# Performance work log

Hardware: AMD Instinct MI355X
Metric: run time of the kernel (lower is better)

Reference implementation:

```python
import jax, jax.numpy as jnp
import numpy as np

EPS = 1e-5  # eqx.nn.LayerNorm default


def _layer_norm(x, w, b):
    m = x.mean(-1, keepdims=True)
    v = ((x - m) ** 2).mean(-1, keepdims=True)
    return (x - m) / jnp.sqrt(v + EPS) * w + b


def _s4_block(x, nw, nb, lre, lim, bre, bim, cre, cim, d, lstep, ow, ob, o2w, o2b):
    # x: [L, H]. One SequenceBlock: LayerNorm -> S4 recurrence (lax.scan) -> GELU -> GLU-style gated linear -> residual.
    skip = x
    h = _layer_norm(x, nw, nb)
    Lam = lre + 1j * lim                      # [H, N] complex diagonal state matrix
    step = jnp.exp(lstep)[:, None]            # [H, 1] per-channel timescale
    BL = 1.0 / (1.0 - (step / 2.0) * Lam)     # bilinear discretization
    Abar = BL * (1.0 + (step / 2.0) * Lam)    # [H, N]
    Bbar = BL * step * (bre + 1j * bim)       # [H, N]
    C = cre + 1j * cim                        # [H, N]

    def scan_fn(state, u):                    # state: [H, N] complex, u: [H]
        new = Abar * state + Bbar * u[:, None]
        y = 2.0 * jnp.sum(C * new, axis=-1).real + d * u
        return new, y

    init = jnp.zeros(Abar.shape, Abar.dtype)  # cell.init_state
    _, y = jax.lax.scan(scan_fn, init, h)     # [L, H]
    y = jax.nn.gelu(y)
    y = (y @ ow.T + ob) * jax.nn.sigmoid(y @ o2w.T + o2b)
    return skip + y


def setup_inputs() -> dict:
    key = jax.random.key(0)
    L, IN, OUT, H, N, NL = 2048, 4, 3, 512, 32, 4
    ks = jax.random.split(key, 16)
    return {
        "x": jax.random.normal(ks[0], (L, IN), jnp.float32),
        "enc_w": jax.random.normal(ks[1], (H, IN), jnp.float32) / np.sqrt(IN),
        "enc_b": jnp.zeros((H,), jnp.float32),
        "dec_w": jax.random.normal(ks[2], (OUT, H), jnp.float32) / np.sqrt(H),
        "dec_b": jnp.zeros((OUT,), jnp.float32),
        "norm_w": jnp.ones((NL, H), jnp.float32),
        "norm_b": jnp.zeros((NL, H), jnp.float32),
        "lam_re": -0.5 - jax.random.uniform(ks[3], (NL, H, N), jnp.float32),  # stable (Re < 0)
        "lam_im": np.pi * jax.random.normal(ks[4], (NL, H, N), jnp.float32),
        "b_re": jax.random.normal(ks[5], (NL, H, N), jnp.float32) / np.sqrt(N),
        "b_im": jax.random.normal(ks[6], (NL, H, N), jnp.float32) / np.sqrt(N),
        "c_re": jax.random.normal(ks[7], (NL, H, N), jnp.float32) / np.sqrt(N),
        "c_im": jax.random.normal(ks[8], (NL, H, N), jnp.float32) / np.sqrt(N),
        "d": jax.random.normal(ks[9], (NL, H), jnp.float32),
        "log_step": float(np.log(1e-3)) + float(np.log(1e-1) - np.log(1e-3)) * jax.random.uniform(ks[10], (NL, H), jnp.float32),
        "out_w": jax.random.normal(ks[11], (NL, H, H), jnp.float32) / np.sqrt(H),
        "out_b": jnp.zeros((NL, H), jnp.float32),
        "out2_w": jax.random.normal(ks[12], (NL, H, H), jnp.float32) / np.sqrt(H),
        "out2_b": jnp.zeros((NL, H), jnp.float32),
    }


def reference(x, enc_w, enc_b, dec_w, dec_b, norm_w, norm_b, lam_re, lam_im, b_re, b_im, c_re, c_im, d, log_step, out_w, out_b, out2_w, out2_b):
    h = x @ enc_w.T + enc_b                   # encoder: [L, IN] -> [L, H]
    for i in range(norm_w.shape[0]):          # fixed small n_layers loop
        h = _s4_block(h, norm_w[i], norm_b[i], lam_re[i], lam_im[i], b_re[i], b_im[i],
                      c_re[i], c_im[i], d[i], log_step[i], out_w[i], out_b[i], out2_w[i], out2_b[i])
    return h @ dec_w.T + dec_b                # decoder: [L, H] -> [L, OUT]
```

## Files before the change

### kernel.cpp

```cpp
#include <hip/hip_runtime.h>
#include <hip/hip_bf16.h>
#include <math.h>

#define LSEQ 2048
#define HD   512
#define NST  32
#define LC   32
#define NCHK 64
#define NSUP 8
#define HH   (HD * HD)

typedef __bf16 bf16;
typedef __bf16 bf16x8 __attribute__((ext_vector_type(8)));
typedef float  floatx4 __attribute__((ext_vector_type(4)));

__device__ __forceinline__ float gelu_tanh(float x) {
    float z = 0.7978845608028654f * (x + 0.044715f * x * x * x);
    float e = __expf(2.f * z);
    float th = 1.f - 2.f / (e + 1.f);
    return 0.5f * x * (1.f + th);
}

__device__ __forceinline__ void make_ab(float lre, float lim, float step,
                                        float br0, float bi0,
                                        float& ar, float& ai, float& br, float& bi) {
    float s2 = 0.5f * step;
    float dr = 1.f - s2 * lre, di = -s2 * lim;
    float inv = 1.f / (dr * dr + di * di);
    float blr = dr * inv, bli = -di * inv;
    float nr = 1.f + s2 * lre, ni = s2 * lim;
    ar = blr * nr - bli * ni;
    ai = blr * ni + bli * nr;
    float tr = step * br0, ti = step * bi0;
    br = blr * tr - bli * ti;
    bi = blr * ti + bli * tr;
}

__global__ __launch_bounds__(256) void setup_kernel(
    const float* __restrict__ x,   const float* __restrict__ ew,
    const float* __restrict__ eb,  const float* __restrict__ ow,
    const float* __restrict__ o2w,
    const float* __restrict__ lre, const float* __restrict__ lim,
    const float* __restrict__ bre, const float* __restrict__ bim,
    const float* __restrict__ cre, const float* __restrict__ cim,
    const float* __restrict__ ls,
    float* __restrict__ h, bf16* __restrict__ wb,
    float2* __restrict__ cA, float2* __restrict__ cB,
    float2* __restrict__ cC, float2* __restrict__ cAp,
    float2* __restrict__ cApJ, float2* __restrict__ statP) {
    int bid = blockIdx.x, tid = threadIdx.x;
    if (bid < 4096) {
        int idx = bid * 256 + tid;
        int t = idx >> 9, col = idx & (HD - 1);
        float4 xv = *(const float4*)(x + t * 4);
        float4 wv = *(const float4*)(ew + col * 4);
        float acc = eb[col];
        acc = fmaf(xv.x, wv.x, acc); acc = fmaf(xv.y, wv.y, acc);
        acc = fmaf(xv.z, wv.z, acc); acc = fmaf(xv.w, wv.w, acc);
        h[idx] = acc;
        float s = acc, s2 = acc * acc;
#pragma unroll
        for (int m = 1; m <= 8; m <<= 1) {
            s  += __shfl_xor(s, m, 64);
            s2 += __shfl_xor(s2, m, 64);
        }
        if ((tid & 15) == 0) statP[(size_t)t * 32 + (col >> 4)] = make_float2(s, s2);
    } else if (bid < 5120) {
        int b2 = bid - 4096;
        const float* src = (b2 >= 512) ? o2w : ow;
        bf16* dst = wb + (b2 >= 512 ? 4 * HH : 0);
        int i = ((b2 & 511) * 256 + tid) * 8;
        float4 a = *(const float4*)(src + i);
        float4 b = *(const float4*)(src + i + 4);
        bf16x8 o;
        o[0] = (bf16)a.x; o[1] = (bf16)a.y; o[2] = (bf16)a.z; o[3] = (bf16)a.w;
        o[4] = (bf16)b.x; o[5] = (bf16)b.y; o[6] = (bf16)b.z; o[7] = (bf16)b.w;
        *(bf16x8*)(dst + i) = o;
    } else {
        int tg = (bid - 5120) * 256 + tid;
        int lay = tg >> 14, rem = tg & 16383;
        int ch = rem >> 5, n = rem & 31;
        float step = __expf(ls[lay * HD + ch]);
        float ar, ai, br, bi;
        make_ab(lre[tg], lim[tg], step, bre[tg], bim[tg], ar, ai, br, bi);
        float xr = ar, xi = ai;
#pragma unroll
        for (int q = 0; q < 5; ++q) { float tt = xr * xr - xi * xi; xi = 2.f * xr * xi; xr = tt; }
        int dst = (lay * NST + n) * HD + ch;
        cA[dst]  = make_float2(ar, ai);
        cB[dst]  = make_float2(br, bi);
        cC[dst]  = make_float2(2.f * cre[tg], 2.f * cim[tg]);
        cAp[dst] = make_float2(xr, xi);
        float pr = xr, pi = xi;
#pragma unroll
        for (int jj = 0; jj < 7; ++jj) {
            cApJ[((size_t)(lay * 7 + jj) * NST + n) * HD + ch] = make_float2(pr, pi);
            float t2r = pr * xr - pi * xi;
            float t2i = pr * xi + pi * xr;
            pr = t2r; pi = t2i;
        }
    }
}

__global__ __launch_bounds__(512, 1) void p1_kernel(
    const float* __restrict__ h, const float2* __restrict__ statP,
    const float* __restrict__ nwp, const float* __restrict__ nbp,
    const float2* __restrict__ cA, const float2* __restrict__ cB,
    const float2* __restrict__ cAp,
    float2* __restrict__ f, int lay) {
    __shared__ float tile[256 * 16];
    __shared__ float2 stat_s[256];
    __shared__ float2 fs[8 * 32 * 16];
    const int tid = threadIdx.x;
    const int lane = tid & 63, w = tid >> 6;
    const int chl = lane & 15, sub = lane >> 4;
    const int bx = blockIdx.x, sup = blockIdx.y;
    const int ch = bx * 16 + chl;

    const float* ub = h + (size_t)(sup * 256) * HD + bx * 16;
#pragma unroll
    for (int r = 0; r < 2; ++r) {
        int i = r * 512 + tid;
        int tr = i >> 2, c4 = (i & 3) * 4;
        *(float4*)(tile + tr * 16 + c4) = *(const float4*)(ub + (size_t)tr * HD + c4);
    }
    if (tid < 256) {
        const float4* pp = (const float4*)(statP + (size_t)(sup * 256 + tid) * 32);
        float S = 0.f, S2 = 0.f;
#pragma unroll
        for (int k = 0; k < 16; ++k) {
            float4 v = pp[k];
            S += v.x + v.z; S2 += v.y + v.w;
        }
        float m = S * (1.f / HD);
        float var = S2 * (1.f / HD) - m * m;
        stat_s[tid] = make_float2(m, rsqrtf(var + 1e-5f));
    }
    int cbase = (lay * NST + sub * 8) * HD + ch;
    float aR[8], aI[8], bR[8], bI[8];
#pragma unroll
    for (int j = 0; j < 8; ++j) {
        float2 t2 = cA[cbase + j * HD]; aR[j] = t2.x; aI[j] = t2.y;
        t2 = cB[cbase + j * HD];        bR[j] = t2.x; bI[j] = t2.y;
    }
    float gam = nwp[ch], bet = nbp[ch];
    __syncthreads();

    const float* tp = tile + (w * 32) * 16 + chl;
    float sr[8], si[8];
#pragma unroll
    for (int j = 0; j < 8; ++j) { sr[j] = 0.f; si[j] = 0.f; }
#pragma unroll 4
    for (int t = 0; t < LC; ++t) {
        float2 st = stat_s[w * 32 + t];
        float gr = gam * st.y;
        float off = fmaf(-st.x, gr, bet);
        float uu = fmaf(tp[t * 16], gr, off);
#pragma unroll
        for (int j = 0; j < 8; ++j) {
            float nr = fmaf(aR[j], sr[j], fmaf(-aI[j], si[j], bR[j] * uu));
            float ni = fmaf(aI[j], sr[j], fmaf( aR[j], si[j], bI[j] * uu));
            sr[j] = nr; si[j] = ni;
        }
    }
#pragma unroll
    for (int j = 0; j < 8; ++j)
        fs[(w * 32 + sub * 8 + j) * 16 + chl] = make_float2(sr[j], si[j]);
    __syncthreads();

    int n2 = tid >> 4, c2 = tid & 15;
    int chg = bx * 16 + c2;
    float2 ap = cAp[(lay * NST + n2) * HD + chg];
    const size_t CS = (size_t)NST * HD;
    float2* fo = f + (size_t)n2 * HD + chg;
    float s2r = 0.f, s2i = 0.f;
#pragma unroll
    for (int k = 0; k < 8; ++k) {
        float2 v = fs[(k * 32 + n2) * 16 + c2];
        float nr = fmaf(ap.x, s2r, fmaf(-ap.y, s2i, v.x));
        float ni = fmaf(ap.y, s2r, fmaf( ap.x, s2i, v.y));
        s2r = nr; s2i = ni;
        fo[(size_t)(sup * 8 + k) * CS] = make_float2(s2r, s2i);
    }
}

__global__ __launch_bounds__(256) void p2_kernel(
    const float2* __restrict__ f, const float2* __restrict__ cAp,
    float2* __restrict__ Sx, int lay) {
    int tg = blockIdx.x * 256 + threadIdx.x;
    int ch = tg & 511, n = tg >> 9;
    float2 ap = cAp[(lay * NST + n) * HD + ch];
    float xr = ap.x, xi = ap.y;
#pragma unroll
    for (int q = 0; q < 3; ++q) { float tt = xr * xr - xi * xi; xi = 2.f * xr * xi; xr = tt; }
    const size_t CS = (size_t)NST * HD;
    const float2* fp = f + (size_t)n * HD + ch;
    float2 F[8];
#pragma unroll
    for (int k = 0; k < 8; ++k) F[k] = fp[(size_t)(k * 8 + 7) * CS];
    float2* sp = Sx + (size_t)n * HD + ch;
    float sr = 0.f, si = 0.f;
#pragma unroll
    for (int k = 0; k < 8; ++k) {
        sp[(size_t)k * CS] = make_float2(sr, si);
        float nr = fmaf(xr, sr, fmaf(-xi, si, F[k].x));
        float ni = fmaf(xi, sr, fmaf( xr, si, F[k].y));
        sr = nr; si = ni;
    }
}

__global__ __launch_bounds__(256, 2) void p3_kernel(
    const float* __restrict__ h, const float2* __restrict__ statP,
    const float* __restrict__ nwp, const float* __restrict__ nbp,
    const float2* __restrict__ f, const float2* __restrict__ Sx,
    const float2* __restrict__ cApJ,
    const float2* __restrict__ cA, const float2* __restrict__ cB,
    const float2* __restrict__ cC, const float* __restrict__ d_p,
    bf16* __restrict__ g, int lay) {
    __shared__ float tile[128 * 16];
    __shared__ float2 stat_s[128];
    const int tid = threadIdx.x;
    const int lane = tid & 63, w = tid >> 6;
    const int chl = lane & 15, sub = lane >> 4;
    const int bx = blockIdx.x, by = blockIdx.y;
    const int ch = bx * 16 + chl;
    const int chunk = by * 4 + w;

    const float* ub = h + (size_t)(by * 128) * HD + bx * 16;
#pragma unroll
    for (int r = 0; r < 2; ++r) {
        int i = r * 256 + tid;
        int tr = i >> 2, c4 = (i & 3) * 4;
        *(float4*)(tile + tr * 16 + c4) = *(const float4*)(ub + (size_t)tr * HD + c4);
    }
    if (tid < 128) {
        const float4* pp = (const float4*)(statP + (size_t)(by * 128 + tid) * 32);
        float S = 0.f, S2 = 0.f;
#pragma unroll
        for (int k = 0; k < 16; ++k) {
            float4 v = pp[k];
            S += v.x + v.z; S2 += v.y + v.w;
        }
        float m = S * (1.f / HD);
        float var = S2 * (1.f / HD) - m * m;
        stat_s[tid] = make_float2(m, rsqrtf(var + 1e-5f));
    }
    int cbase = (lay * NST + sub * 8) * HD + ch;
    float aR[8], aI[8], bR[8], bI[8], cR[8], cI[8];
#pragma unroll
    for (int j = 0; j < 8; ++j) {
        float2 t2 = cA[cbase + j * HD]; aR[j] = t2.x; aI[j] = t2.y;
        t2 = cB[cbase + j * HD];        bR[j] = t2.x; bI[j] = t2.y;
        t2 = cC[cbase + j * HD];        cR[j] = t2.x; cI[j] = t2.y;
    }
    float dch = d_p[lay * HD + ch];
    float gam = nwp[ch], bet = nbp[ch];

    float sr[8], si[8];
    int jj = chunk & 7, ksup = chunk >> 3;
    if (chunk == 0) {
#pragma unroll
        for (int j = 0; j < 8; ++j) { sr[j] = 0.f; si[j] = 0.f; }
    } else if (jj == 0) {
        const float2* sp = Sx + ((size_t)ksup * NST + sub * 8) * HD + ch;
#pragma unroll
        for (int j = 0; j < 8; ++j) { float2 v = sp[(size_t)j * HD]; sr[j] = v.x; si[j] = v.y; }
    } else {
        const float2* fw = f + ((size_t)(chunk - 1) * NST + sub * 8) * HD + ch;
        const float2* sp = Sx + ((size_t)ksup * NST + sub * 8) * HD + ch;
        const float2* aj = cApJ + ((size_t)(lay * 7 + (jj - 1)) * NST + sub * 8) * HD + ch;
#pragma unroll
        for (int j = 0; j < 8; ++j) {
            float2 F = fw[(size_t)j * HD];
            float2 S = sp[(size_t)j * HD];
            float2 A = aj[(size_t)j * HD];
            sr[j] = fmaf(A.x, S.x, fmaf(-A.y, S.y, F.x));
            si[j] = fmaf(A.x, S.y, fmaf( A.y, S.x, F.y));
        }
    }
    __syncthreads();

    const float* tp = tile + (w * 32) * 16 + chl;
    bf16* gp = g + (size_t)chunk * LC * HD + ch;
#pragma unroll 4
    for (int t = 0; t < LC; ++t) {
        float2 st = stat_s[w * 32 + t];
        float gr = gam * st.y;
        float off = fmaf(-st.x, gr, bet);
        float uu = fmaf(tp[t * 16], gr, off);
        float p = 0.f;
#pragma unroll
        for (int j = 0; j < 8; ++j) {
            float nr = fmaf(aR[j], sr[j], fmaf(-aI[j], si[j], bR[j] * uu));
            float ni = fmaf(aI[j], sr[j], fmaf( aR[j], si[j], bI[j] * uu));
            sr[j] = nr; si[j] = ni;
            p = fmaf(cR[j], nr, fmaf(-cI[j], ni, p));
        }
        p += __shfl_xor(p, 16);
        p += __shfl_xor(p, 32);
        float y = fmaf(dch, uu, p);
        if (sub == 0) gp[(size_t)t * HD] = (bf16)gelu_tanh(y);
    }
}

__global__ __launch_bounds__(256, 2) void mm_kernel(
    const bf16* __restrict__ A,
    const bf16* __restrict__ W1,
    const bf16* __restrict__ W2,
    const float* __restrict__ bias1, const float* __restrict__ bias2,
    float* __restrict__ Hio, float2* __restrict__ statP, int doStats) {
    const int w = threadIdx.x >> 6, lane = threadIdx.x & 63;
    const int wm = w >> 1, wn = w & 1;
    const int bm = blockIdx.x >> 4, bn = blockIdx.x & 15;
    const int mW = bm * 64 + wm * 32;
    const int nW = bn * 32 + wn * 16;
    const int lrow = lane & 15, quad = lane >> 4;

    floatx4 acc1[2] = {{0.f,0.f,0.f,0.f},{0.f,0.f,0.f,0.f}};
    floatx4 acc2[2] = {{0.f,0.f,0.f,0.f},{0.f,0.f,0.f,0.f}};
    for (int k0 = 0; k0 < HD; k0 += 32) {
        int kk = k0 + quad * 8;
        bf16x8 a0 = *(const bf16x8*)(A + (size_t)(mW + lrow) * HD + kk);
        bf16x8 a1 = *(const bf16x8*)(A + (size_t)(mW + 16 + lrow) * HD + kk);
        bf16x8 p0 = *(const bf16x8*)(W1 + (size_t)(nW + lrow) * HD + kk);
        bf16x8 q0 = *(const bf16x8*)(W2 + (size_t)(nW + lrow) * HD + kk);
        acc1[0] = __builtin_amdgcn_mfma_f32_16x16x32_bf16(a0, p0, acc1[0], 0, 0, 0);
        acc1[1] = __builtin_amdgcn_mfma_f32_16x16x32_bf16(a1, p0, acc1[1], 0, 0, 0);
        acc2[0] = __builtin_amdgcn_mfma_f32_16x16x32_bf16(a0, q0, acc2[0], 0, 0, 0);
        acc2[1] = __builtin_amdgcn_mfma_f32_16x16x32_bf16(a1, q0, acc2[1], 0, 0, 0);
    }
    int jj = nW + lrow;
    float bb1 = bias1[jj], bb2 = bias2[jj];
    float hn_[2][4];
#pragma unroll
    for (int fm = 0; fm < 2; ++fm)
#pragma unroll
        for (int r = 0; r < 4; ++r) {
            int t = mW + fm * 16 + quad * 4 + r;
            float z1 = acc1[fm][r] + bb1;
            float z2 = acc2[fm][r] + bb2;
            float v = Hio[(size_t)t * HD + jj] + z1 / (1.f + __expf(-z2));
            Hio[(size_t)t * HD + jj] = v;
            hn_[fm][r] = v;
        }
    if (doStats) {
#pragma unroll
        for (int fm = 0; fm < 2; ++fm)
#pragma unroll
            for (int r = 0; r < 4; ++r) {
                float s = hn_[fm][r], s2 = s * s;
#pragma unroll
                for (int m = 1; m <= 8; m <<= 1) {
                    s  += __shfl_xor(s, m, 64);
                    s2 += __shfl_xor(s2, m, 64);
                }
                if (lrow == 0) {
                    int t = mW + fm * 16 + quad * 4 + r;
                    statP[(size_t)t * 32 + (nW >> 4)] = make_float2(s, s2);
                }
            }
    }
}

__global__ __launch_bounds__(192) void dec_kernel(
    const float* __restrict__ h, const float* __restrict__ w,
    const float* __restrict__ b, float* __restrict__ out) {
    int j = threadIdx.x >> 6, lane = threadIdx.x & 63;
    int t = blockIdx.x;
    const float* hp = h + (size_t)t * HD + lane * 8;
    float v[8];
    *(float4*)(v)     = *(const float4*)(hp);
    *(float4*)(v + 4) = *(const float4*)(hp + 4);
    float w8[8];
    *(float4*)(w8)     = *(const float4*)(w + j * HD + lane * 8);
    *(float4*)(w8 + 4) = *(const float4*)(w + j * HD + lane * 8 + 4);
    float s = 0.f;
#pragma unroll
    for (int e = 0; e < 8; ++e) s = fmaf(v[e], w8[e], s);
#pragma unroll
    for (int m = 32; m; m >>= 1) s += __shfl_xor(s, m, 64);
    if (lane == 0) out[t * 3 + j] = s + b[j];
}

extern "C" void kernel_launch(void* const* d_in, const int* in_sizes, int n_in,
                              void* d_out, int out_size, void* d_ws, size_t ws_size,
                              hipStream_t stream) {
    const float* x   = (const float*)d_in[0];
    const float* ew  = (const float*)d_in[1];
    const float* eb  = (const float*)d_in[2];
    const float* dw  = (const float*)d_in[3];
    const float* db  = (const float*)d_in[4];
    const float* nw  = (const float*)d_in[5];
    const float* nb  = (const float*)d_in[6];
    const float* lre = (const float*)d_in[7];
    const float* lim = (const float*)d_in[8];
    const float* bre = (const float*)d_in[9];
    const float* bim = (const float*)d_in[10];
    const float* cre = (const float*)d_in[11];
    const float* cim = (const float*)d_in[12];
    const float* dd  = (const float*)d_in[13];
    const float* ls  = (const float*)d_in[14];
    const float* ow  = (const float*)d_in[15];
    const float* ob  = (const float*)d_in[16];
    const float* o2w = (const float*)d_in[17];
    const float* o2b = (const float*)d_in[18];

    char* ws = (char*)d_ws;
    float*  h     = (float*)ws;
    float2* f     = (float2*)(ws + (4  << 20));
    bf16*   g     = (bf16*)(ws + (16 << 20));
    bf16*   wb    = (bf16*)(ws + (18 << 20));
    float2* cA    = (float2*)(ws + (22 << 20));
    float2* cB    = (float2*)(ws + (22 << 20) + (512 << 10));
    float2* cC    = (float2*)(ws + (23 << 20));
    float2* cAp   = (float2*)(ws + (23 << 20) + (512 << 10));
    float2* statP = (float2*)(ws + (24 << 20));
    float2* cApJ  = (float2*)(ws + (25 << 20));
    float2* Sx    = (float2*)(ws + (29 << 20));

    setup_kernel<<<5376, 256, 0, stream>>>(x, ew, eb, ow, o2w,
                                           lre, lim, bre, bim, cre, cim, ls,
                                           h, wb, cA, cB, cC, cAp, cApJ, statP);
    for (int lay = 0; lay < 4; ++lay) {
        int oH = lay * HD;
        p1_kernel<<<dim3(HD / 16, NSUP), 512, 0, stream>>>(
            h, statP, nw + oH, nb + oH, cA, cB, cAp, f, lay);
        p2_kernel<<<64, 256, 0, stream>>>(f, cAp, Sx, lay);
        p3_kernel<<<dim3(HD / 16, NCHK / 4), 256, 0, stream>>>(
            h, statP, nw + oH, nb + oH, f, Sx, cApJ, cA, cB, cC, dd, g, lay);
        mm_kernel<<<512, 256, 0, stream>>>(
            g, wb + lay * HH, wb + 4 * HH + lay * HH, ob + oH, o2b + oH, h,
            statP, lay < 3 ? 1 : 0);
    }
    dec_kernel<<<LSEQ, 192, 0, stream>>>(h, dw, db, (float*)d_out);
}
```

Measured before the change: 308.3 us.

## Halve scan chunk length and GEMM tile to double parallelism across kernels

The chunked S4 scan now uses chunks of 16 timesteps instead of 32, giving 128 chunks and 16 super-chunks. Chunk-state powers drop from A^32 to A^16, and the p1, p2 and p3 tiles and launch bounds are adjusted to match. The bf16 MFMA GEMM tile is halved in M so it launches 1024 blocks with higher occupancy hints. This aims to fill more compute units on short, latency-bound kernels, at the cost of more partial states, a longer serial p2 carry, and less A reuse in the GEMM.

Result: slower. 327.0 us (+6.1%).

```diff
diff --git a/kernel.cpp b/kernel.cpp
--- a/kernel.cpp
+++ b/kernel.cpp
@@ -5,9 +5,10 @@
 #define LSEQ 2048
 #define HD   512
 #define NST  32
-#define LC   32
-#define NCHK 64
-#define NSUP 8
+#define LC   16
+#define NCHK 128
+#define SUP  8
+#define NSUP 16
 #define HH   (HD * HD)
 
 typedef __bf16 bf16;
@@ -85,7 +86,7 @@
         make_ab(lre[tg], lim[tg], step, bre[tg], bim[tg], ar, ai, br, bi);
         float xr = ar, xi = ai;
 #pragma unroll
-        for (int q = 0; q < 5; ++q) { float tt = xr * xr - xi * xi; xi = 2.f * xr * xi; xr = tt; }
+        for (int q = 0; q < 4; ++q) { float tt = xr * xr - xi * xi; xi = 2.f * xr * xi; xr = tt; }
         int dst = (lay * NST + n) * HD + ch;
         cA[dst]  = make_float2(ar, ai);
         cB[dst]  = make_float2(br, bi);
@@ -102,14 +103,14 @@
     }
 }
 
-__global__ __launch_bounds__(512, 1) void p1_kernel(
+__global__ __launch_bounds__(512, 4) void p1_kernel(
     const float* __restrict__ h, const float2* __restrict__ statP,
     const float* __restrict__ nwp, const float* __restrict__ nbp,
     const float2* __restrict__ cA, const float2* __restrict__ cB,
     const float2* __restrict__ cAp,
     float2* __restrict__ f, int lay) {
-    __shared__ float tile[256 * 16];
-    __shared__ float2 stat_s[256];
+    __shared__ float tile[128 * 16];
+    __shared__ float2 stat_s[128];
     __shared__ float2 fs[8 * 32 * 16];
     const int tid = threadIdx.x;
     const int lane = tid & 63, w = tid >> 6;
@@ -117,15 +118,13 @@
     const int bx = blockIdx.x, sup = blockIdx.y;
     const int ch = bx * 16 + chl;
 
-    const float* ub = h + (size_t)(sup * 256) * HD + bx * 16;
-#pragma unroll
-    for (int r = 0; r < 2; ++r) {
-        int i = r * 512 + tid;
-        int tr = i >> 2, c4 = (i & 3) * 4;
+    const float* ub = h + (size_t)(sup * 128) * HD + bx * 16;
+    {
+        int tr = tid >> 2, c4 = (tid & 3) * 4;
         *(float4*)(tile + tr * 16 + c4) = *(const float4*)(ub + (size_t)tr * HD + c4);
     }
-    if (tid < 256) {
-        const float4* pp = (const float4*)(statP + (size_t)(sup * 256 + tid) * 32);
+    if (tid < 128) {
+        const float4* pp = (const float4*)(statP + (size_t)(sup * 128 + tid) * 32);
         float S = 0.f, S2 = 0.f;
 #pragma unroll
         for (int k = 0; k < 16; ++k) {
@@ -146,13 +145,13 @@
     float gam = nwp[ch], bet = nbp[ch];
     __syncthreads();
 
-    const float* tp = tile + (w * 32) * 16 + chl;
+    const float* tp = tile + (w * LC) * 16 + chl;
     float sr[8], si[8];
 #pragma unroll
     for (int j = 0; j < 8; ++j) { sr[j] = 0.f; si[j] = 0.f; }
 #pragma unroll 4
     for (int t = 0; t < LC; ++t) {
-        float2 st = stat_s[w * 32 + t];
+        float2 st = stat_s[w * LC + t];
         float gr = gam * st.y;
         float off = fmaf(-st.x, gr, bet);
         float uu = fmaf(tp[t * 16], gr, off);
@@ -195,13 +194,13 @@
     for (int q = 0; q < 3; ++q) { float tt = xr * xr - xi * xi; xi = 2.f * xr * xi; xr = tt; }
     const size_t CS = (size_t)NST * HD;
     const float2* fp = f + (size_t)n * HD + ch;
-    float2 F[8];
-#pragma unroll
-    for (int k = 0; k < 8; ++k) F[k] = fp[(size_t)(k * 8 + 7) * CS];
+    float2 F[NSUP];
+#pragma unroll
+    for (int k = 0; k < NSUP; ++k) F[k] = fp[(size_t)(k * 8 + 7) * CS];
     float2* sp = Sx + (size_t)n * HD + ch;
     float sr = 0.f, si = 0.f;
 #pragma unroll
-    for (int k = 0; k < 8; ++k) {
+    for (int k = 0; k < NSUP; ++k) {
         sp[(size_t)k * CS] = make_float2(sr, si);
         float nr = fmaf(xr, sr, fmaf(-xi, si, F[k].x));
         float ni = fmaf(xi, sr, fmaf( xr, si, F[k].y));
@@ -209,7 +208,7 @@
     }
 }
 
-__global__ __launch_bounds__(256, 2) void p3_kernel(
+__global__ __launch_bounds__(256, 4) void p3_kernel(
     const float* __restrict__ h, const float2* __restrict__ statP,
     const float* __restrict__ nwp, const float* __restrict__ nbp,
     const float2* __restrict__ f, const float2* __restrict__ Sx,
@@ -217,8 +216,8 @@
     const float2* __restrict__ cA, const float2* __restrict__ cB,
     const float2* __restrict__ cC, const float* __restrict__ d_p,
     bf16* __restrict__ g, int lay) {
-    __shared__ float tile[128 * 16];
-    __shared__ float2 stat_s[128];
+    __shared__ float tile[64 * 16];
+    __shared__ float2 stat_s[64];
     const int tid = threadIdx.x;
     const int lane = tid & 63, w = tid >> 6;
     const int chl = lane & 15, sub = lane >> 4;
@@ -226,15 +225,13 @@
     const int ch = bx * 16 + chl;
     const int chunk = by * 4 + w;
 
-    const float* ub = h + (size_t)(by * 128) * HD + bx * 16;
-#pragma unroll
-    for (int r = 0; r < 2; ++r) {
-        int i = r * 256 + tid;
-        int tr = i >> 2, c4 = (i & 3) * 4;
+    const float* ub = h + (size_t)(by * 64) * HD + bx * 16;
+    {
+        int tr = tid >> 2, c4 = (tid & 3) * 4;
         *(float4*)(tile + tr * 16 + c4) = *(const float4*)(ub + (size_t)tr * HD + c4);
     }
-    if (tid < 128) {
-        const float4* pp = (const float4*)(statP + (size_t)(by * 128 + tid) * 32);
+    if (tid < 64) {
+        const float4* pp = (const float4*)(statP + (size_t)(by * 64 + tid) * 32);
         float S = 0.f, S2 = 0.f;
 #pragma unroll
         for (int k = 0; k < 16; ++k) {
@@ -280,11 +277,11 @@
     }
     __syncthreads();
 
-    const float* tp = tile + (w * 32) * 16 + chl;
+    const float* tp = tile + (w * LC) * 16 + chl;
     bf16* gp = g + (size_t)chunk * LC * HD + ch;
 #pragma unroll 4
     for (int t = 0; t < LC; ++t) {
-        float2 st = stat_s[w * 32 + t];
+        float2 st = stat_s[w * LC + t];
         float gr = gam * st.y;
         float off = fmaf(-st.x, gr, bet);
         float uu = fmaf(tp[t * 16], gr, off);
@@ -303,7 +300,7 @@
     }
 }
 
-__global__ __launch_bounds__(256, 2) void mm_kernel(
+__global__ __launch_bounds__(256, 4) void mm_kernel(
     const bf16* __restrict__ A,
     const bf16* __restrict__ W1,
     const bf16* __restrict__ W2,
@@ -312,53 +309,46 @@
     const int w = threadIdx.x >> 6, lane = threadIdx.x & 63;
     const int wm = w >> 1, wn = w & 1;
     const int bm = blockIdx.x >> 4, bn = blockIdx.x & 15;
-    const int mW = bm * 64 + wm * 32;
+    const int mW = bm * 32 + wm * 16;
     const int nW = bn * 32 + wn * 16;
     const int lrow = lane & 15, quad = lane >> 4;
 
-    floatx4 acc1[2] = {{0.f,0.f,0.f,0.f},{0.f,0.f,0.f,0.f}};
-    floatx4 acc2[2] = {{0.f,0.f,0.f,0.f},{0.f,0.f,0.f,0.f}};
+    floatx4 acc1 = {0.f, 0.f, 0.f, 0.f};
+    floatx4 acc2 = {0.f, 0.f, 0.f, 0.f};
     for (int k0 = 0; k0 < HD; k0 += 32) {
         int kk = k0 + quad * 8;
         bf16x8 a0 = *(const bf16x8*)(A + (size_t)(mW + lrow) * HD + kk);
-        bf16x8 a1 = *(const bf16x8*)(A + (size_t)(mW + 16 + lrow) * HD + kk);
         bf16x8 p0 = *(const bf16x8*)(W1 + (size_t)(nW + lrow) * HD + kk);
         bf16x8 q0 = *(const bf16x8*)(W2 + (size_t)(nW + lrow) * HD + kk);
-        acc1[0] = __builtin_amdgcn_mfma_f32_16x16x32_bf16(a0, p0, acc1[0], 0, 0, 0);
-        acc1[1] = __builtin_amdgcn_mfma_f32_16x16x32_bf16(a1, p0, acc1[1], 0, 0, 0);
-        acc2[0] = __builtin_amdgcn_mfma_f32_16x16x32_bf16(a0, q0, acc2[0], 0, 0, 0);
-        acc2[1] = __builtin_amdgcn_mfma_f32_16x16x32_bf16(a1, q0, acc2[1], 0, 0, 0);
+        acc1 = __builtin_amdgcn_mfma_f32_16x16x32_bf16(a0, p0, acc1, 0, 0, 0);
+        acc2 = __builtin_amdgcn_mfma_f32_16x16x32_bf16(a0, q0, acc2, 0, 0, 0);
     }
     int jj = nW + lrow;
     float bb1 = bias1[jj], bb2 = bias2[jj];
-    float hn_[2][4];
-#pragma unroll
-    for (int fm = 0; fm < 2; ++fm)
+    float hn_[4];
+#pragma unroll
+    for (int r = 0; r < 4; ++r) {
+        int t = mW + quad * 4 + r;
+        float z1 = acc1[r] + bb1;
+        float z2 = acc2[r] + bb2;
+        float v = Hio[(size_t)t * HD + jj] + z1 / (1.f + __expf(-z2));
+        Hio[(size_t)t * HD + jj] = v;
+        hn_[r] = v;
+    }
+    if (doStats) {
 #pragma unroll
         for (int r = 0; r < 4; ++r) {
-            int t = mW + fm * 16 + quad * 4 + r;
-            float z1 = acc1[fm][r] + bb1;
-            float z2 = acc2[fm][r] + bb2;
-            float v = Hio[(size_t)t * HD + jj] + z1 / (1.f + __expf(-z2));
-            Hio[(size_t)t * HD + jj] = v;
-            hn_[fm][r] = v;
-        }
-    if (doStats) {
-#pragma unroll
-        for (int fm = 0; fm < 2; ++fm)
-#pragma unroll
-            for (int r = 0; r < 4; ++r) {
-                float s = hn_[fm][r], s2 = s * s;
-#pragma unroll
-                for (int m = 1; m <= 8; m <<= 1) {
-                    s  += __shfl_xor(s, m, 64);
-                    s2 += __shfl_xor(s2, m, 64);
-                }
-                if (lrow == 0) {
-                    int t = mW + fm * 16 + quad * 4 + r;
-                    statP[(size_t)t * 32 + (nW >> 4)] = make_float2(s, s2);
-                }
+            float s = hn_[r], s2 = s * s;
+#pragma unroll
+            for (int m = 1; m <= 8; m <<= 1) {
+                s  += __shfl_xor(s, m, 64);
+                s2 += __shfl_xor(s2, m, 64);
             }
+            if (lrow == 0) {
+                int t = mW + quad * 4 + r;
+                statP[(size_t)t * 32 + (nW >> 4)] = make_float2(s, s2);
+            }
+        }
     }
 }
 
@@ -408,15 +398,15 @@
     char* ws = (char*)d_ws;
     float*  h     = (float*)ws;
     float2* f     = (float2*)(ws + (4  << 20));
-    bf16*   g     = (bf16*)(ws + (16 << 20));
-    bf16*   wb    = (bf16*)(ws + (18 << 20));
-    float2* cA    = (float2*)(ws + (22 << 20));
-    float2* cB    = (float2*)(ws + (22 << 20) + (512 << 10));
-    float2* cC    = (float2*)(ws + (23 << 20));
-    float2* cAp   = (float2*)(ws + (23 << 20) + (512 << 10));
-    float2* statP = (float2*)(ws + (24 << 20));
-    float2* cApJ  = (float2*)(ws + (25 << 20));
-    float2* Sx    = (float2*)(ws + (29 << 20));
+    bf16*   g     = (bf16*)(ws + (21 << 20));
+    bf16*   wb    = (bf16*)(ws + (23 << 20));
+    float2* cA    = (float2*)(ws + (27 << 20));
+    float2* cB    = (float2*)(ws + (27 << 20) + (512 << 10));
+    float2* cC    = (float2*)(ws + (28 << 20));
+    float2* cAp   = (float2*)(ws + (28 << 20) + (512 << 10));
+    float2* statP = (float2*)(ws + (29 << 20));
+    float2* cApJ  = (float2*)(ws + (30 << 20));
+    float2* Sx    = (float2*)(ws + (34 << 20));
 
     setup_kernel<<<5376, 256, 0, stream>>>(x, ew, eb, ow, o2w,
                                            lre, lim, bre, bim, cre, cim, ls,
@@ -428,7 +418,7 @@
         p2_kernel<<<64, 256, 0, stream>>>(f, cAp, Sx, lay);
         p3_kernel<<<dim3(HD / 16, NCHK / 4), 256, 0, stream>>>(
             h, statP, nw + oH, nb + oH, f, Sx, cApJ, cA, cB, cC, dd, g, lay);
-        mm_kernel<<<512, 256, 0, stream>>>(
+        mm_kernel<<<1024, 256, 0, stream>>>(
             g, wb + lay * HH, wb + 4 * HH + lay * HH, ob + oH, o2b + oH, h,
             statP, lay < 3 ? 1 : 0);
     }
```
